# Optimization experiments

Measured on AMD Instinct MI355X. Metric: run time of the kernel, lower is better.

## Reference

```python
import jax, jax.numpy as jnp
import numpy as np

N_NODES = 100000
N_EDGES = 3200000
N_TYPES = 118
N_PARAMS = 22
CUTOFF = 8.0


def _default_eta_mu():
    # eta = 4.5 constant, mu linearly spaced from 7.5 down to 0.5 (22 values),
    # same set of parameters for every of the 118 atom types.
    mu = np.linspace(7.5, 0.5, N_PARAMS, dtype=np.float32)
    eta = np.full_like(mu, 4.5)
    table = np.stack([eta, mu], axis=-1)  # [22, 2]
    return jnp.asarray(np.broadcast_to(table, (N_TYPES, N_PARAMS, 2)).copy())


def setup_inputs() -> dict:
    key = jax.random.key(0)
    k1, k2, k3 = jax.random.split(key, 3)
    z = jax.random.randint(k1, (N_NODES,), 0, N_TYPES, dtype=jnp.int32)
    # coordinates spread out so r_ij spans the [0, cutoff] range realistically
    xyz = jax.random.normal(k2, (N_NODES, 3), dtype=jnp.float32) * 4.0
    eij = jax.random.randint(k3, (N_EDGES, 2), 0, N_NODES, dtype=jnp.int32)
    eta_mu = _default_eta_mu()
    return {"z": z, "xyz": xyz, "eij": eij, "eta_mu": eta_mu}


def reference(z, xyz, eij, eta_mu):
    recv = eij[:, 0]  # i (ingoing / receiver)
    send = eij[:, 1]  # j (outgoing / sender)
    xi = xyz[recv]                      # [M, 3]
    xj = xyz[send]                      # [M, 3]
    rij = jnp.sqrt(jnp.sum(jnp.square(xi - xj), axis=-1, keepdims=True))  # [M, 1]
    # cosine cutoff f_c(r)
    fc = 0.5 * (jnp.cos(jnp.clip(rij, -CUTOFF, CUTOFF) * (np.pi / CUTOFF)) + 1.0)  # [M, 1]
    # per-receiver-type Gaussian expansion
    params = eta_mu[z[recv]]            # [M, 22, 2]
    eta = params[..., 0]                # [M, 22]
    mu = params[..., 1]                 # [M, 22]
    gij = jnp.exp(-eta * jnp.square(rij - mu))  # [M, 22]
    # weight g(Z_j) = atomic number of sender
    w = z[send].astype(xyz.dtype)[:, None]      # [M, 1]
    rep = gij * fc * w                  # [M, 22]
    return jax.ops.segment_sum(rep, recv, num_segments=z.shape[0])  # [N, 22]
```

## Files before the change

### kernel.cpp

```cpp
#include <hip/hip_runtime.h>
#include <math.h>

#define N_NODES  100000
#define N_EDGES  3200000
#define N_TYPES  118
#define N_PARAMS 22
#define CUTOFF   8.0f
#define PI_OVER_CUT 0.39269908169872415f

#define CAP 48
#define NPART 8
#define NODES_PER_PART ((N_NODES + NPART - 1) / NPART)
#define BUCKET_GRID 2048

#define SCAN_ITEMS 1024
#define SCAN_NBLK  ((N_NODES + SCAN_ITEMS - 1) / SCAN_ITEMS)


__global__ __launch_bounds__(256) void k_pack(
    const int* __restrict__ z, const float* __restrict__ xyz,
    float4* __restrict__ xyzw, int* __restrict__ counts)
{
    const int n = blockIdx.x * 256 + threadIdx.x;
    if (n >= N_NODES) return;
    counts[n] = 0;
    xyzw[n] = make_float4(xyz[3*n+0], xyz[3*n+1], xyz[3*n+2], (float)z[n]);
}

__global__ __launch_bounds__(256) void k_bucket_part(
    const float4* __restrict__ xyzw, const int* __restrict__ eij,
    int* __restrict__ counts, float2* __restrict__ buckets)
{
    const int part = blockIdx.x & (NPART - 1);
    const int grp  = blockIdx.x >> 3;
    const int ngrp = gridDim.x  >> 3;
    const int lo = part * NODES_PER_PART;
    const int hi = lo + NODES_PER_PART;

    const int tid0   = grp * 256 + threadIdx.x;
    const int stride = ngrp * 256;

    for (int e = tid0; e < N_EDGES; e += stride) {
        const int2 pr = ((const int2*)eij)[e];
        const int r = pr.x;
        if (r < lo || r >= hi) continue;
        const float4 a = xyzw[r];
        const float4 b = xyzw[pr.y];
        const float dx = a.x - b.x, dy = a.y - b.y, dz = a.z - b.z;
        const float rij = sqrtf(dx*dx + dy*dy + dz*dz);
        const int   wz  = (int)b.w;
        if (rij < CUTOFF && wz != 0) {
            const float fc  = 0.5f * (cosf(rij * PI_OVER_CUT) + 1.0f);
            const int slot  = atomicAdd(&counts[r], 1);
            if (slot < CAP)
                buckets[(size_t)r * CAP + slot] = make_float2(rij, (float)wz * fc);
        }
    }
}

__global__ __launch_bounds__(256) void k_acc3(
    const int* __restrict__ z, const float* __restrict__ eta_mu,
    const int* __restrict__ counts, const float2* __restrict__ buckets,
    float* __restrict__ out)
{
    const int tid  = blockIdx.x * 256 + threadIdx.x;
    const int node = tid >> 5;
    const int lane = tid & 31;
    if (node >= N_NODES) return;

    const int cnt = min(counts[node], CAP);
    const float2* __restrict__ row = buckets + (size_t)node * CAP;

    float2 v0 = make_float2(0.0f, 0.0f);
    float2 v1 = make_float2(0.0f, 0.0f);
    if (lane < cnt)      v0 = row[lane];
    if (lane + 32 < cnt) v1 = row[lane + 32];

    float eta = 0.0f, mu = 0.0f;
    if (lane < N_PARAMS) {
        const int t = z[node] * N_PARAMS + lane;
        eta = eta_mu[2*t + 0];
        mu  = eta_mu[2*t + 1];
    }

    float acc = 0.0f;
    const int c0 = min(cnt, 32);
    for (int e = 0; e < c0; ++e) {
        const float rx = __shfl(v0.x, e, 32);
        const float wy = __shfl(v0.y, e, 32);
        const float d  = rx - mu;
        acc += wy * __expf(-eta * d * d);
    }
    if (cnt > 32) {
        const int c1 = cnt - 32;
        for (int e = 0; e < c1; ++e) {
            const float rx = __shfl(v1.x, e, 32);
            const float wy = __shfl(v1.y, e, 32);
            const float d  = rx - mu;
            acc += wy * __expf(-eta * d * d);
        }
    }

    if (lane < N_PARAMS)
        out[(size_t)node * N_PARAMS + lane] = acc;
}


__global__ __launch_bounds__(256) void k_count(
    const int* __restrict__ z, const float* __restrict__ xyz,
    const int* __restrict__ eij, int* __restrict__ counts)
{
    int e = blockIdx.x * 256 + threadIdx.x;
    if (e >= N_EDGES) return;
    const int2 p = ((const int2*)eij)[e];
    const float dx = xyz[3*p.x+0] - xyz[3*p.y+0];
    const float dy = xyz[3*p.x+1] - xyz[3*p.y+1];
    const float dz = xyz[3*p.x+2] - xyz[3*p.y+2];
    const float rij = sqrtf(dx*dx + dy*dy + dz*dz);
    if (rij >= CUTOFF) return;
    if (z[p.y] == 0) return;
    atomicAdd(&counts[p.x], 1);
}

__global__ __launch_bounds__(256) void k_scanA(
    const int* __restrict__ counts, int* __restrict__ blockSums)
{
    __shared__ int s[256];
    const int base = blockIdx.x * SCAN_ITEMS;
    int sum = 0;
    for (int i = threadIdx.x; i < SCAN_ITEMS; i += 256) {
        int idx = base + i;
        sum += (idx < N_NODES) ? counts[idx] : 0;
    }
    s[threadIdx.x] = sum;
    __syncthreads();
    for (int o = 128; o > 0; o >>= 1) {
        if (threadIdx.x < o) s[threadIdx.x] += s[threadIdx.x + o];
        __syncthreads();
    }
    if (threadIdx.x == 0) blockSums[blockIdx.x] = s[0];
}

__global__ void k_scanB(int* __restrict__ blockSums, int* __restrict__ offsets)
{
    if (threadIdx.x == 0 && blockIdx.x == 0) {
        int run = 0;
        for (int i = 0; i < SCAN_NBLK; ++i) {
            int v = blockSums[i];
            blockSums[i] = run;
            run += v;
        }
        offsets[N_NODES] = run;
    }
}

__global__ __launch_bounds__(256) void k_scanC(
    const int* __restrict__ counts, const int* __restrict__ blockSums,
    int* __restrict__ offsets, int* __restrict__ cursor)
{
    __shared__ int s[256];
    const int base = blockIdx.x * SCAN_ITEMS + threadIdx.x * 4;
    int v[4];
    int tsum = 0;
#pragma unroll
    for (int j = 0; j < 4; ++j) {
        int idx = base + j;
        v[j] = (idx < N_NODES) ? counts[idx] : 0;
        tsum += v[j];
    }
    s[threadIdx.x] = tsum;
    __syncthreads();
    for (int o = 1; o < 256; o <<= 1) {
        int t = 0;
        if ((int)threadIdx.x >= o) t = s[threadIdx.x - o];
        __syncthreads();
        s[threadIdx.x] += t;
        __syncthreads();
    }
    int run = s[threadIdx.x] - tsum + blockSums[blockIdx.x];
#pragma unroll
    for (int j = 0; j < 4; ++j) {
        int idx = base + j;
        if (idx < N_NODES) { offsets[idx] = run; cursor[idx] = run; }
        run += v[j];
    }
}

__global__ __launch_bounds__(256) void k_scatter(
    const int* __restrict__ z, const float* __restrict__ xyz,
    const int* __restrict__ eij, int* __restrict__ cursor,
    float2* __restrict__ compact)
{
    int e = blockIdx.x * 256 + threadIdx.x;
    if (e >= N_EDGES) return;
    const int2 p = ((const int2*)eij)[e];
    const float dx = xyz[3*p.x+0] - xyz[3*p.y+0];
    const float dy = xyz[3*p.x+1] - xyz[3*p.y+1];
    const float dz = xyz[3*p.x+2] - xyz[3*p.y+2];
    const float rij = sqrtf(dx*dx + dy*dy + dz*dz);
    if (rij >= CUTOFF) return;
    const int wz = z[p.y];
    if (wz == 0) return;
    const float fc  = 0.5f * (cosf(rij * PI_OVER_CUT) + 1.0f);
    const float wfc = (float)wz * fc;
    const int slot = atomicAdd(&cursor[p.x], 1);
    compact[slot] = make_float2(rij, wfc);
}

__global__ __launch_bounds__(256) void k_acc(
    const int* __restrict__ z, const float* __restrict__ eta_mu,
    const int* __restrict__ offsets, const float2* __restrict__ compact,
    float* __restrict__ out)
{
    __shared__ float s_eta[N_TYPES * N_PARAMS];
    __shared__ float s_mu [N_TYPES * N_PARAMS];
    for (int i = threadIdx.x; i < N_TYPES * N_PARAMS; i += 256) {
        s_eta[i] = eta_mu[2*i + 0];
        s_mu [i] = eta_mu[2*i + 1];
    }
    __syncthreads();

    const int n = blockIdx.x * 256 + threadIdx.x;
    if (n >= N_NODES) return;

    const int beg = offsets[n];
    const int end = offsets[n + 1];
    const int t   = z[n] * N_PARAMS;

    float acc[N_PARAMS];
#pragma unroll
    for (int p = 0; p < N_PARAMS; ++p) acc[p] = 0.0f;

    for (int e = beg; e < end; ++e) {
        const float2 v = compact[e];
#pragma unroll
        for (int p = 0; p < N_PARAMS; ++p) {
            const float d = v.x - s_mu[t + p];
            acc[p] += v.y * __expf(-s_eta[t + p] * d * d);
        }
    }

    float* __restrict__ o = out + (size_t)n * N_PARAMS;
#pragma unroll
    for (int p = 0; p < N_PARAMS; ++p) o[p] = acc[p];
}


__global__ __launch_bounds__(256) void wacsf_edge_kernel(
    const int* __restrict__ z, const float* __restrict__ xyz,
    const int* __restrict__ eij, const float* __restrict__ eta_mu,
    float* __restrict__ out)
{
    __shared__ float s_eta[N_TYPES * N_PARAMS];
    __shared__ float s_mu [N_TYPES * N_PARAMS];
    for (int i = threadIdx.x; i < N_TYPES * N_PARAMS; i += blockDim.x) {
        s_eta[i] = eta_mu[2*i + 0];
        s_mu [i] = eta_mu[2*i + 1];
    }
    __syncthreads();
    int e = blockIdx.x * blockDim.x + threadIdx.x;
    if (e >= N_EDGES) return;
    const int2 pair = ((const int2*)eij)[e];
    const float dx = xyz[3*pair.x+0] - xyz[3*pair.y+0];
    const float dy = xyz[3*pair.x+1] - xyz[3*pair.y+1];
    const float dz = xyz[3*pair.x+2] - xyz[3*pair.y+2];
    const float rij = sqrtf(dx*dx + dy*dy + dz*dz);
    if (rij >= CUTOFF) return;
    const float w = (float)z[pair.y];
    if (w == 0.0f) return;
    const float fc  = 0.5f * (cosf(rij * PI_OVER_CUT) + 1.0f);
    const float wfc = w * fc;
    const int t = z[pair.x] * N_PARAMS;
    float* __restrict__ o = out + (size_t)pair.x * N_PARAMS;
#pragma unroll
    for (int p = 0; p < N_PARAMS; ++p) {
        const float d = rij - s_mu[t + p];
        atomicAdd(&o[p], wfc * __expf(-s_eta[t + p] * d * d));
    }
}

extern "C" void kernel_launch(void* const* d_in, const int* in_sizes, int n_in,
                              void* d_out, int out_size, void* d_ws, size_t ws_size,
                              hipStream_t stream) {
    const int*   z      = (const int*)  d_in[0];
    const float* xyz    = (const float*)d_in[1];
    const int*   eij    = (const int*)  d_in[2];
    const float* eta_mu = (const float*)d_in[3];
    float* out = (float*)d_out;
    char* ws = (char*)d_ws;

    {
        size_t off = 0;
        auto take = [&](size_t bytes) -> size_t {
            size_t cur = off;
            off = (off + bytes + 255) & ~(size_t)255;
            return cur;
        };
        const size_t o_counts  = take((size_t)N_NODES * 4);
        const size_t o_xyzw    = take((size_t)N_NODES * 16);
        const size_t o_buckets = take((size_t)N_NODES * CAP * 8);
        if (ws_size >= off) {
            int*    counts  = (int*)   (ws + o_counts);
            float4* xyzw    = (float4*)(ws + o_xyzw);
            float2* buckets = (float2*)(ws + o_buckets);
            const int ngrid = (N_NODES + 255) / 256;
            k_pack<<<ngrid, 256, 0, stream>>>(z, xyz, xyzw, counts);
            k_bucket_part<<<BUCKET_GRID, 256, 0, stream>>>(xyzw, eij, counts, buckets);
            const long long accThreads = (long long)N_NODES * 32;
            k_acc3<<<(int)((accThreads + 255) / 256), 256, 0, stream>>>(
                z, eta_mu, counts, buckets, out);
            return;
        }
    }

    {
        size_t off = 0;
        auto take = [&](size_t bytes) -> size_t {
            size_t cur = off;
            off = (off + bytes + 255) & ~(size_t)255;
            return cur;
        };
        const size_t o_counts  = take((size_t)N_NODES * 4);
        const size_t o_cursor  = take((size_t)N_NODES * 4);
        const size_t o_offsets = take((size_t)(N_NODES + 1) * 4);
        const size_t o_bsums   = take((size_t)SCAN_NBLK * 4);
        const size_t o_compact = take((size_t)N_EDGES * 8);
        if (ws_size >= off) {
            int*    counts  = (int*)   (ws + o_counts);
            int*    cursor  = (int*)   (ws + o_cursor);
            int*    offsets = (int*)   (ws + o_offsets);
            int*    bsums   = (int*)   (ws + o_bsums);
            float2* compact = (float2*)(ws + o_compact);
            (void)hipMemsetAsync(counts, 0, (size_t)N_NODES * 4, stream);
            const int egrid = (N_EDGES + 255) / 256;
            k_count  <<<egrid, 256, 0, stream>>>(z, xyz, eij, counts);
            k_scanA  <<<SCAN_NBLK, 256, 0, stream>>>(counts, bsums);
            k_scanB  <<<1, 64, 0, stream>>>(bsums, offsets);
            k_scanC  <<<SCAN_NBLK, 256, 0, stream>>>(counts, bsums, offsets, cursor);
            k_scatter<<<egrid, 256, 0, stream>>>(z, xyz, eij, cursor, compact);
            k_acc    <<<(N_NODES + 255) / 256, 256, 0, stream>>>(z, eta_mu, offsets, compact, out);
            return;
        }
    }

    (void)hipMemsetAsync(out, 0, (size_t)out_size * sizeof(float), stream);
    wacsf_edge_kernel<<<(N_EDGES + 255) / 256, 256, 0, stream>>>(z, xyz, eij, eta_mu, out);
}
```

Measured before the change: 192.5 us.

## Replace partitioned edge bucketing with one-pass grid and padded per-node counters

Drops the 8-way receiver-range partitioning, where every block group re-read the whole edge list, and launches one thread per edge with nontemporal index loads. Per-node atomic counters are padded to a 64-byte stride to avoid atomic contention between neighbouring nodes sharing a cache line. This trades the locality of bucket writes and atomics within a partition for reading the edge list only once, and adds a larger counter array.

```diff
diff --git a/kernel.cpp b/kernel.cpp
--- a/kernel.cpp
+++ b/kernel.cpp
@@ -9,9 +9,7 @@
 #define PI_OVER_CUT 0.39269908169872415f
 
 #define CAP 48
-#define NPART 8
-#define NODES_PER_PART ((N_NODES + NPART - 1) / NPART)
-#define BUCKET_GRID 2048
+#define CSTRIDE 16
 
 #define SCAN_ITEMS 1024
 #define SCAN_NBLK  ((N_NODES + SCAN_ITEMS - 1) / SCAN_ITEMS)
@@ -23,38 +21,32 @@
 {
     const int n = blockIdx.x * 256 + threadIdx.x;
     if (n >= N_NODES) return;
-    counts[n] = 0;
+    counts[(size_t)n * CSTRIDE] = 0;
     xyzw[n] = make_float4(xyz[3*n+0], xyz[3*n+1], xyz[3*n+2], (float)z[n]);
 }
 
-__global__ __launch_bounds__(256) void k_bucket_part(
+__global__ __launch_bounds__(256) void k_bucket(
     const float4* __restrict__ xyzw, const int* __restrict__ eij,
     int* __restrict__ counts, float2* __restrict__ buckets)
 {
-    const int part = blockIdx.x & (NPART - 1);
-    const int grp  = blockIdx.x >> 3;
-    const int ngrp = gridDim.x  >> 3;
-    const int lo = part * NODES_PER_PART;
-    const int hi = lo + NODES_PER_PART;
-
-    const int tid0   = grp * 256 + threadIdx.x;
-    const int stride = ngrp * 256;
-
-    for (int e = tid0; e < N_EDGES; e += stride) {
-        const int2 pr = ((const int2*)eij)[e];
-        const int r = pr.x;
-        if (r < lo || r >= hi) continue;
-        const float4 a = xyzw[r];
-        const float4 b = xyzw[pr.y];
-        const float dx = a.x - b.x, dy = a.y - b.y, dz = a.z - b.z;
-        const float rij = sqrtf(dx*dx + dy*dy + dz*dz);
-        const int   wz  = (int)b.w;
-        if (rij < CUTOFF && wz != 0) {
-            const float fc  = 0.5f * (cosf(rij * PI_OVER_CUT) + 1.0f);
-            const int slot  = atomicAdd(&counts[r], 1);
-            if (slot < CAP)
-                buckets[(size_t)r * CAP + slot] = make_float2(rij, (float)wz * fc);
-        }
+    const int e = blockIdx.x * 256 + threadIdx.x;
+    if (e >= N_EDGES) return;
+
+    const int r = __builtin_nontemporal_load(eij + 2*(size_t)e + 0);
+    const int s = __builtin_nontemporal_load(eij + 2*(size_t)e + 1);
+
+    const float4 a = xyzw[r];
+    const float4 b = xyzw[s];
+    const float dx = a.x - b.x, dy = a.y - b.y, dz = a.z - b.z;
+    const float rij = sqrtf(dx*dx + dy*dy + dz*dz);
+    const int   wz  = (int)b.w;
+
+    if (rij < CUTOFF && wz != 0) {
+        const float fc  = 0.5f * (cosf(rij * PI_OVER_CUT) + 1.0f);
+        const float wfc = (float)wz * fc;
+        const int slot  = atomicAdd(&counts[(size_t)r * CSTRIDE], 1);
+        if (slot < CAP)
+            buckets[(size_t)r * CAP + slot] = make_float2(rij, wfc);
     }
 }
 
@@ -68,7 +60,7 @@
     const int lane = tid & 31;
     if (node >= N_NODES) return;
 
-    const int cnt = min(counts[node], CAP);
+    const int cnt = min(counts[(size_t)node * CSTRIDE], CAP);
     const float2* __restrict__ row = buckets + (size_t)node * CAP;
 
     float2 v0 = make_float2(0.0f, 0.0f);
@@ -296,7 +288,7 @@
             off = (off + bytes + 255) & ~(size_t)255;
             return cur;
         };
-        const size_t o_counts  = take((size_t)N_NODES * 4);
+        const size_t o_counts  = take((size_t)N_NODES * CSTRIDE * 4);
         const size_t o_xyzw    = take((size_t)N_NODES * 16);
         const size_t o_buckets = take((size_t)N_NODES * CAP * 8);
         if (ws_size >= off) {
@@ -305,7 +297,7 @@
             float2* buckets = (float2*)(ws + o_buckets);
             const int ngrid = (N_NODES + 255) / 256;
             k_pack<<<ngrid, 256, 0, stream>>>(z, xyz, xyzw, counts);
-            k_bucket_part<<<BUCKET_GRID, 256, 0, stream>>>(xyzw, eij, counts, buckets);
+            k_bucket<<<(N_EDGES + 255) / 256, 256, 0, stream>>>(xyzw, eij, counts, buckets);
             const long long accThreads = (long long)N_NODES * 32;
             k_acc3<<<(int)((accThreads + 255) / 256), 256, 0, stream>>>(
                 z, eta_mu, counts, buckets, out);
```

Result: slower. 198.4 us (+3.1%).
